# Optimization experiments

Hardware: AMD Instinct MI355X
Metric: run time of the kernel (lower is better)

The kernel has to match this reference:

```python
import jax, jax.numpy as jnp
import numpy as np

# dims (match init_kwargs / input_specs)
B, T = 32, 512
DIM, DEPTH, HEADS, NB_FEAT, N_MASKS = 256, 6, 8, 128, 4
DIM_HEAD = DIM // HEADS  # 32
FF_MULT = 4
KERNEL_EPS = 1e-4


def _orth_proj(key, m, d):
    # FAVOR+ gaussian orthogonal random features: stacked QR blocks, row norms from fresh gaussians
    nb = m // d
    keys = jax.random.split(key, nb + 1)
    blocks = []
    for i in range(nb):
        g = jax.random.normal(keys[i], (d, d))
        q, _ = jnp.linalg.qr(g)
        blocks.append(q.T)
    proj = jnp.concatenate(blocks, axis=0)  # (m, d)
    norms = jnp.linalg.norm(jax.random.normal(keys[-1], (m, d)), axis=-1)
    return (proj * norms[:, None]).astype(jnp.float32)


def setup_inputs() -> dict:
    key = jax.random.key(0)
    ks = jax.random.split(key, 12)
    init = lambda k, sh: (jax.random.normal(k, sh, dtype=jnp.float32) * 0.02)
    L = DEPTH
    return {
        "mel": jax.random.normal(ks[0], (B, DIM, T), dtype=jnp.float32),
        "proj": _orth_proj(ks[1], NB_FEAT, DIM_HEAD),
        "ln1_g": jnp.ones((L, DIM), jnp.float32), "ln1_b": jnp.zeros((L, DIM), jnp.float32),
        "Wq": init(ks[2], (L, DIM, DIM)), "Wk": init(ks[3], (L, DIM, DIM)),
        "Wv": init(ks[4], (L, DIM, DIM)),
        "Wo": init(ks[5], (L, DIM, DIM)), "bo": jnp.zeros((L, DIM), jnp.float32),
        "ln2_g": jnp.ones((L, DIM), jnp.float32), "ln2_b": jnp.zeros((L, DIM), jnp.float32),
        "W1": init(ks[6], (L, DIM, FF_MULT * DIM)), "b1": jnp.zeros((L, FF_MULT * DIM), jnp.float32),
        "W2": init(ks[7], (L, FF_MULT * DIM, DIM)), "b2": jnp.zeros((L, DIM), jnp.float32),
        "Wm": init(ks[8], (DIM, N_MASKS)), "bm": jnp.zeros((N_MASKS,), jnp.float32),
    }


def _ln(x, g, b):
    mu = jnp.mean(x, -1, keepdims=True)
    var = jnp.var(x, -1, keepdims=True)
    return (x - mu) * jax.lax.rsqrt(var + 1e-5) * g + b


def _softmax_kernel(x, proj, is_query):
    # x: (B,H,N,dh), proj: (m,dh)
    dn = x.shape[-1] ** -0.25
    ratio = proj.shape[0] ** -0.5
    xd = jnp.einsum('bhnd,md->bhnm', x * dn, proj)
    diag = 0.5 * jnp.sum(jnp.square(x * dn), axis=-1, keepdims=True)
    if is_query:
        mx = jnp.max(xd, axis=-1, keepdims=True)
    else:
        mx = jnp.max(xd, axis=(-1, -2), keepdims=True)
    return ratio * (jnp.exp(xd - diag - mx) + KERNEL_EPS)


def _split_heads(x):
    b, n, _ = x.shape
    return x.reshape(b, n, HEADS, DIM_HEAD).transpose(0, 2, 1, 3)  # (B,H,N,dh)


def _forward(mel, proj, ln1_g, ln1_b, Wq, Wk, Wv, Wo, bo, ln2_g, ln2_b, W1, b1, W2, b2, Wm, bm):
    x = jnp.transpose(mel, (0, 2, 1))  # (B, T, DIM)
    for l in range(DEPTH):
        # --- FAVOR+ self-attention (pre-LN, non-causal linear attention) ---
        h = _ln(x, ln1_g[l], ln1_b[l])
        q = _split_heads(h @ Wq[l])
        k = _split_heads(h @ Wk[l])
        v = _split_heads(h @ Wv[l])
        qp = _softmax_kernel(q, proj, True)   # (B,H,T,m)
        kp = _softmax_kernel(k, proj, False)  # (B,H,T,m)
        ctx = jnp.einsum('bhnm,bhnd->bhmd', kp, v)          # (B,H,m,dh)
        o = jnp.einsum('bhnm,bhmd->bhnd', qp, ctx)          # (B,H,T,dh)
        denom = jnp.einsum('bhnm,bhm->bhn', qp, kp.sum(axis=2))
        o = o / denom[..., None]
        o = o.transpose(0, 2, 1, 3).reshape(x.shape[0], x.shape[1], DIM)
        x = x + o @ Wo[l] + bo[l]
        h = _ln(x, ln2_g[l], ln2_b[l])
        x = x + jax.nn.gelu(h @ W1[l] + b1[l]) @ W2[l] + b2[l]
    masks = x @ Wm + bm                  # (B, T, M)
    return jnp.transpose(masks, (0, 2, 1))  # (B, M, T)


def reference(mel, proj, ln1_g, ln1_b, Wq, Wk, Wv, Wo, bo, ln2_g, ln2_b, W1, b1, W2, b2, Wm, bm):
    return _forward(mel, proj, ln1_g, ln1_b, Wq, Wk, Wv, Wo, bo, ln2_g, ln2_b, W1, b1, W2, b2, Wm, bm)
```

## Files before the change

kernel.cpp:

```cpp
#include <hip/hip_runtime.h>
#include <math.h>

#define B 32
#define T 512
#define D 256
#define H 8
#define DH 32
#define MF 128
#define NLAYER 6
#define FF 1024
#define NM 4
#define BT (B*T)
#define BH (B*H)

#define DN2H 0.08838834764831845f
#define DNS  0.4204482076268573f
#define RATIO 0.08838834764831845f
#define KEPS 1e-4f

typedef __attribute__((ext_vector_type(8))) short short8;
typedef __attribute__((ext_vector_type(4))) float f32x4;

#define MFMA(a, b, c) __builtin_amdgcn_mfma_f32_16x16x32_bf16(a, b, c, 0, 0, 0)

#define SWZG(l) (((((l) & 3) + (((l) >> 3) & 3)) & 3) * 8)
#define RS(li, gi) (((((gi) - ((li) >> 1)) & 3)) * 8)

#define WAIT_VM(N) asm volatile("s_waitcnt vmcnt(" #N ")" ::: "memory")

__device__ __forceinline__ ushort f2b(float x) {
  union { float f; unsigned u; } c; c.f = x;
  unsigned r = (c.u + 0x7FFFu + ((c.u >> 16) & 1u)) >> 16;
  return (ushort)r;
}
__device__ __forceinline__ float bf2f(ushort u) {
  union { unsigned u; float f; } c; c.u = ((unsigned)u) << 16;
  return c.f;
}
__device__ __forceinline__ void gload16(const ushort* g, ushort* l) {
  __builtin_amdgcn_global_load_lds((const __attribute__((address_space(1))) void*)g,
                                   (__attribute__((address_space(3))) void*)l, 16, 0, 0);
}

__global__ void transpose_mel(const float* __restrict__ mel, float* __restrict__ x) {
  __shared__ float tile[32][33];
  int b = blockIdx.z;
  int d0 = blockIdx.y * 32, t0 = blockIdx.x * 32;
  int tx = threadIdx.x, ty = threadIdx.y;
  #pragma unroll
  for (int i = 0; i < 32; i += 8)
    tile[ty + i][tx] = mel[(b * D + d0 + ty + i) * T + t0 + tx];
  __syncthreads();
  #pragma unroll
  for (int i = 0; i < 32; i += 8)
    x[(b * T + t0 + ty + i) * D + d0 + tx] = tile[tx][ty + i];
}

__global__ void wtrans(const float* __restrict__ W, ushort* __restrict__ WT,
                       int K, int N, size_t lin, size_t lout) {
  __shared__ float tile[32][33];
  int l = blockIdx.z;
  const float* Wl = W + (size_t)l * lin;
  ushort* WTl = WT + (size_t)l * lout;
  int k0 = blockIdx.y * 32, n0 = blockIdx.x * 32;
  int tx = threadIdx.x, ty = threadIdx.y;
  #pragma unroll
  for (int i = 0; i < 32; i += 8)
    tile[ty + i][tx] = Wl[(size_t)(k0 + ty + i) * N + n0 + tx];
  __syncthreads();
  #pragma unroll
  for (int i = 0; i < 32; i += 8)
    WTl[(size_t)(n0 + ty + i) * K + k0 + tx] = f2b(tile[tx][ty + i]);
}

__global__ void proj_conv(const float* __restrict__ proj, ushort* __restrict__ projd) {
  int e = blockIdx.x * 256 + threadIdx.x;
  if (e < MF * DH) projd[e] = f2b(proj[e] * DNS);
}

__global__ __launch_bounds__(256) void ln_kernel(const float* __restrict__ x, const float* __restrict__ g,
                          const float* __restrict__ bb, ushort* __restrict__ y) {
  int row = blockIdx.x * 4 + (threadIdx.x >> 6);
  int lane = threadIdx.x & 63;
  const float4 v = ((const float4*)(x + (size_t)row * D))[lane];
  float s = v.x + v.y + v.z + v.w;
  #pragma unroll
  for (int off = 32; off; off >>= 1) s += __shfl_down(s, off);
  s = __shfl(s, 0);
  float mu = s * (1.0f / 256.0f);
  float dx = v.x - mu, dy = v.y - mu, dz = v.z - mu, dw = v.w - mu;
  float q = dx * dx + dy * dy + dz * dz + dw * dw;
  #pragma unroll
  for (int off = 32; off; off >>= 1) q += __shfl_down(q, off);
  q = __shfl(q, 0);
  float rstd = rsqrtf(q * (1.0f / 256.0f) + 1e-5f);
  const float4 gg = ((const float4*)g)[lane];
  const float4 be = ((const float4*)bb)[lane];
  ushort4 o;
  o.x = f2b(dx * rstd * gg.x + be.x);
  o.y = f2b(dy * rstd * gg.y + be.y);
  o.z = f2b(dz * rstd * gg.z + be.z);
  o.w = f2b(dw * rstd * gg.w + be.w);
  ((ushort4*)(y + (size_t)row * D))[lane] = o;
}

template<int EPI, int BM>
__global__ __launch_bounds__(256) void gemm_bf16(
    const ushort* __restrict__ A, const ushort* __restrict__ BTm,
    const float* __restrict__ bias,
    ushort* __restrict__ outB,
    ushort* __restrict__ qo, ushort* __restrict__ ko, ushort* __restrict__ vT,
    int N, int K) {
  constexpr int MFR = BM / 32;
  __shared__ __align__(16) ushort Al[2][BM * 32];
  __shared__ __align__(16) ushort Bl[2][128 * 32];
  int tid = threadIdx.x;
  int wave = tid >> 6, lane = tid & 63;
  int wr = wave >> 1, wc = wave & 1;
  int gi = lane >> 4, li = lane & 15;
  int lrow = lane >> 2, lkb = SWZG(lane);
  int row0 = blockIdx.y * BM, col0 = blockIdx.x * 128;
  f32x4 acc[MFR][4] = {};

  auto stage = [&](int buf, int kk) {
    #pragma unroll
    for (int i = 0; i < BM / 64; i++) {
      int chunk = wave * (BM / 64) + i;
      gload16(&A[(size_t)(row0 + chunk * 16 + lrow) * K + kk + lkb], &Al[buf][chunk * 512]);
    }
    #pragma unroll
    for (int i = 0; i < 2; i++) {
      int chunk = wave * 2 + i;
      gload16(&BTm[(size_t)(col0 + chunk * 16 + lrow) * K + kk + lkb], &Bl[buf][chunk * 512]);
    }
  };

  stage(0, 0);
  int cur = 0;
  for (int k0 = 0; k0 < K; k0 += 32, cur ^= 1) {
    if (k0 + 32 < K) {
      stage(cur ^ 1, k0 + 32);
      if (BM == 64) { WAIT_VM(3); } else { WAIT_VM(4); }
    } else {
      WAIT_VM(0);
    }
    __builtin_amdgcn_s_barrier();
    __builtin_amdgcn_sched_barrier(0);
    short8 a[MFR], b[4];
    #pragma unroll
    for (int m = 0; m < MFR; m++)
      a[m] = *(const short8*)&Al[cur][(wr * (MFR * 16) + m * 16 + li) * 32 + RS(li, gi)];
    #pragma unroll
    for (int n = 0; n < 4; n++)
      b[n] = *(const short8*)&Bl[cur][(wc * 64 + n * 16 + li) * 32 + RS(li, gi)];
    #pragma unroll
    for (int m = 0; m < MFR; m++)
      #pragma unroll
      for (int n = 0; n < 4; n++)
        acc[m][n] = MFMA(a[m], b[n], acc[m][n]);
    __builtin_amdgcn_s_barrier();
  }
  #pragma unroll
  for (int m = 0; m < MFR; m++) {
    int rbase = row0 + wr * (MFR * 16) + m * 16 + gi * 4;
    #pragma unroll
    for (int n = 0; n < 4; n++) {
      int col = col0 + wc * 64 + n * 16 + li;
      f32x4 v = acc[m][n];
      if (EPI == 2) {
        float bs = bias[col];
        #pragma unroll
        for (int r = 0; r < 4; r++) {
          float u = v[r] + bs;
          float p = u + 0.044715f * u * u * u;
          float gel = u / (1.0f + __expf(-1.5957691216057308f * p));
          outB[(size_t)(rbase + r) * N + col] = f2b(gel);
        }
      } else {
        if (col < 256) {
          #pragma unroll
          for (int r = 0; r < 4; r++) qo[(size_t)(rbase + r) * 256 + col] = f2b(v[r]);
        } else if (col < 512) {
          #pragma unroll
          for (int r = 0; r < 4; r++) ko[(size_t)(rbase + r) * 256 + col - 256] = f2b(v[r]);
        } else {
          int b_ = rbase >> 9, t = rbase & 511;
          int hh = (col - 512) >> 5, d = (col - 512) & 31;
          ushort4 pk;
          pk.x = f2b(v[0]); pk.y = f2b(v[1]); pk.z = f2b(v[2]); pk.w = f2b(v[3]);
          *(ushort4*)&vT[((size_t)((b_ * 8 + hh) * 32 + d)) * 512 + t] = pk;
        }
      }
    }
  }
}

__global__ __launch_bounds__(256) void ctx_fused(
    const ushort* __restrict__ kb, const ushort* __restrict__ projd,
    const ushort* __restrict__ vT, ushort* __restrict__ Bmat) {
  __shared__ __align__(16) ushort Kl[512 * 32];
  __shared__ __align__(16) ushort Pl[128 * 32];
  __shared__ __align__(16) ushort Sl[2][128 * 40];
  __shared__ __align__(16) ushort Bvl[2][32 * 32];
  __shared__ float dg_s[512];
  __shared__ float red_s[256];
  int bh = blockIdx.x;
  int b = bh >> 3, h = bh & 7;
  int tid = threadIdx.x, wave = tid >> 6, lane = tid & 63;
  int gi = lane >> 4, li = lane & 15;
  int lrow = lane >> 2, lkb = (lane & 3) * 8;
  const ushort* Kg = kb + (size_t)(b * 512) * 256 + h * 32;
  const ushort* Vg = vT + (size_t)bh * 32 * 512;
  #pragma unroll
  for (int i = 0; i < 8; i++) {
    int chunk = wave * 8 + i;
    gload16(&Kg[(size_t)(chunk * 16 + lrow) * 256 + lkb], &Kl[chunk * 512]);
  }
  #pragma unroll
  for (int i = 0; i < 2; i++) {
    int chunk = wave * 2 + i;
    gload16(&projd[(chunk * 16 + lrow) * 32 + lkb], &Pl[chunk * 512]);
  }
  __syncthreads();
  #pragma unroll
  for (int i = 0; i < 2; i++) {
    int t = tid * 2 + i;
    const ushort* kr = &Kl[t * 32];
    float s = 0.f;
    #pragma unroll
    for (int j = 0; j < 32; j++) { float v = bf2f(kr[j]); s += v * v; }
    dg_s[t] = DN2H * s;
  }
  short8 bp0 = *(const short8*)&Pl[(wave * 32 + li) * 32 + gi * 8];
  short8 bp1 = *(const short8*)&Pl[(wave * 32 + 16 + li) * 32 + gi * 8];
  float smax = -1e30f;
  for (int c = 0; c < 16; c++) {
    int t0c = c * 32;
    short8 a0 = *(const short8*)&Kl[(t0c + li) * 32 + gi * 8];
    short8 a1 = *(const short8*)&Kl[(t0c + 16 + li) * 32 + gi * 8];
    f32x4 s00 = {}, s01 = {}, s10 = {}, s11 = {};
    s00 = MFMA(a0, bp0, s00); s01 = MFMA(a0, bp1, s01);
    s10 = MFMA(a1, bp0, s10); s11 = MFMA(a1, bp1, s11);
    #pragma unroll
    for (int r = 0; r < 4; r++)
      smax = fmaxf(smax, fmaxf(fmaxf(s00[r], s01[r]), fmaxf(s10[r], s11[r])));
  }
  red_s[tid] = smax;
  __syncthreads();
  for (int s = 128; s; s >>= 1) {
    if (tid < s) red_s[tid] = fmaxf(red_s[tid], red_s[tid + s]);
    __syncthreads();
  }
  float km = red_s[0];
  f32x4 cacc[2][2] = {};
  float ks0 = 0.f, ks1 = 0.f;
  int cur = 0;
  for (int c = 0; c < 16; c++, cur ^= 1) {
    int t0c = c * 32;
    if (wave < 2)
      gload16(&Vg[(size_t)(wave * 16 + lrow) * 512 + t0c + lkb], &Bvl[cur][wave * 512]);
    short8 a0 = *(const short8*)&Kl[(t0c + li) * 32 + gi * 8];
    short8 a1 = *(const short8*)&Kl[(t0c + 16 + li) * 32 + gi * 8];
    f32x4 s00 = {}, s01 = {}, s10 = {}, s11 = {};
    s00 = MFMA(a0, bp0, s00); s01 = MFMA(a0, bp1, s01);
    s10 = MFMA(a1, bp0, s10); s11 = MFMA(a1, bp1, s11);
    ushort4 w00, w01, w10, w11;
    #pragma unroll
    for (int r = 0; r < 4; r++) {
      float d0 = dg_s[t0c + gi * 4 + r];
      float d1 = dg_s[t0c + 16 + gi * 4 + r];
      float k00 = RATIO * (__expf(s00[r] - d0 - km) + KEPS);
      float k01 = RATIO * (__expf(s01[r] - d0 - km) + KEPS);
      float k10 = RATIO * (__expf(s10[r] - d1 - km) + KEPS);
      float k11 = RATIO * (__expf(s11[r] - d1 - km) + KEPS);
      ks0 += k00 + k10; ks1 += k01 + k11;
      ((ushort*)&w00)[r] = f2b(k00); ((ushort*)&w01)[r] = f2b(k01);
      ((ushort*)&w10)[r] = f2b(k10); ((ushort*)&w11)[r] = f2b(k11);
    }
    *(ushort4*)&Sl[cur][(wave * 32 + li) * 40 + gi * 4]           = w00;
    *(ushort4*)&Sl[cur][(wave * 32 + 16 + li) * 40 + gi * 4]      = w01;
    *(ushort4*)&Sl[cur][(wave * 32 + li) * 40 + 16 + gi * 4]      = w10;
    *(ushort4*)&Sl[cur][(wave * 32 + 16 + li) * 40 + 16 + gi * 4] = w11;
    __syncthreads();
    short8 ca0 = *(const short8*)&Sl[cur][(wave * 32 + li) * 40 + gi * 8];
    short8 ca1 = *(const short8*)&Sl[cur][(wave * 32 + 16 + li) * 40 + gi * 8];
    short8 cb0 = *(const short8*)&Bvl[cur][li * 32 + gi * 8];
    short8 cb1 = *(const short8*)&Bvl[cur][(16 + li) * 32 + gi * 8];
    cacc[0][0] = MFMA(ca0, cb0, cacc[0][0]);
    cacc[0][1] = MFMA(ca0, cb1, cacc[0][1]);
    cacc[1][0] = MFMA(ca1, cb0, cacc[1][0]);
    cacc[1][1] = MFMA(ca1, cb1, cacc[1][1]);
  }
  ks0 += __shfl_xor(ks0, 16); ks0 += __shfl_xor(ks0, 32);
  ks1 += __shfl_xor(ks1, 16); ks1 += __shfl_xor(ks1, 32);
  if (gi == 0) {
    Bmat[((size_t)bh * 48 + 32) * 128 + wave * 32 + li] = f2b(ks0);
    Bmat[((size_t)bh * 48 + 32) * 128 + wave * 32 + 16 + li] = f2b(ks1);
  }
  #pragma unroll
  for (int m = 0; m < 2; m++)
    #pragma unroll
    for (int n = 0; n < 2; n++) {
      int dd = n * 16 + li;
      int mg = wave * 32 + m * 16 + gi * 4;
      ushort4 pk;
      pk.x = f2b(cacc[m][n][0]); pk.y = f2b(cacc[m][n][1]);
      pk.z = f2b(cacc[m][n][2]); pk.w = f2b(cacc[m][n][3]);
      *(ushort4*)&Bmat[((size_t)bh * 48 + dd) * 128 + mg] = pk;
    }
  for (int e = tid; e < 15 * 128; e += 256)
    Bmat[((size_t)bh * 48 + 33) * 128 + e] = 0;
}

__global__ __launch_bounds__(256) void favq_o(
    const ushort* __restrict__ qb, const ushort* __restrict__ projd,
    const ushort* __restrict__ Bmat, ushort* __restrict__ ob) {
  __shared__ __align__(16) ushort Ql[64 * 32];
  __shared__ __align__(16) ushort Pl[128 * 32];
  __shared__ __align__(16) ushort Sl[64 * 136];
  __shared__ __align__(16) ushort Bml[48 * 136];
  __shared__ float dgq[64];
  int bh = blockIdx.y;
  int t0 = blockIdx.x * 64;
  int b = bh >> 3, h = bh & 7;
  int tid = threadIdx.x, wave = tid >> 6, lane = tid & 63;
  int gi = lane >> 4, li = lane & 15;
  int lrow = lane >> 2, lkb = (lane & 3) * 8;
  const ushort* Qg = qb + (size_t)(b * 512) * 256 + h * 32;
  gload16(&Qg[(size_t)(t0 + wave * 16 + lrow) * 256 + lkb], &Ql[wave * 512]);
  #pragma unroll
  for (int i = 0; i < 2; i++) {
    int chunk = wave * 2 + i;
    gload16(&projd[(chunk * 16 + lrow) * 32 + lkb], &Pl[chunk * 512]);
  }
  #pragma unroll
  for (int j = 0; j < 3; j++) {
    int c = j * 256 + tid;
    int r = c >> 4, g = c & 15;
    *(uint4*)&Bml[r * 136 + g * 8] = *(const uint4*)&Bmat[(size_t)bh * 48 * 128 + r * 128 + g * 8];
  }
  __syncthreads();
  if (tid < 64) {
    const ushort* qr = &Ql[tid * 32];
    float s = 0.f;
    #pragma unroll
    for (int j = 0; j < 32; j++) { float v = bf2f(qr[j]); s += v * v; }
    dgq[tid] = DN2H * s;
  }
  short8 bq = *(const short8*)&Ql[(wave * 16 + li) * 32 + gi * 8];
  f32x4 sacc[8] = {};
  #pragma unroll
  for (int m = 0; m < 8; m++) {
    short8 a = *(const short8*)&Pl[(m * 16 + li) * 32 + gi * 8];
    sacc[m] = MFMA(a, bq, sacc[m]);
  }
  __syncthreads();
  float mx = -1e30f;
  #pragma unroll
  for (int m = 0; m < 8; m++)
    #pragma unroll
    for (int r = 0; r < 4; r++) mx = fmaxf(mx, sacc[m][r]);
  mx = fmaxf(mx, __shfl_xor(mx, 16));
  mx = fmaxf(mx, __shfl_xor(mx, 32));
  float dg = dgq[wave * 16 + li];
  #pragma unroll
  for (int m = 0; m < 8; m++) {
    ushort4 o4;
    #pragma unroll
    for (int r = 0; r < 4; r++)
      ((ushort*)&o4)[r] = f2b(RATIO * (__expf(sacc[m][r] - dg - mx) + KEPS));
    *(ushort4*)&Sl[(wave * 16 + li) * 136 + m * 16 + gi * 4] = o4;
  }
  __syncthreads();
  f32x4 oacc[3] = {};
  #pragma unroll
  for (int ks = 0; ks < 4; ks++) {
    short8 a = *(const short8*)&Sl[(wave * 16 + li) * 136 + ks * 32 + gi * 8];
    #pragma unroll
    for (int n = 0; n < 3; n++) {
      short8 bb = *(const short8*)&Bml[(n * 16 + li) * 136 + ks * 32 + gi * 8];
      oacc[n] = MFMA(a, bb, oacc[n]);
    }
  }
  int t = t0 + wave * 16 + gi * 4;
  float den[4];
  #pragma unroll
  for (int r = 0; r < 4; r++) den[r] = __shfl(oacc[2][r], lane & 48);
  #pragma unroll
  for (int n = 0; n < 2; n++)
    #pragma unroll
    for (int r = 0; r < 4; r++)
      ob[((size_t)(b * 512) + t + r) * 256 + h * 32 + n * 16 + li] = f2b(oacc[n][r] / den[r]);
}

__global__ __launch_bounds__(256) void wo_ff1(
    const ushort* __restrict__ ob, const ushort* __restrict__ woT,
    const float* __restrict__ bo, const float* __restrict__ res, float* __restrict__ x,
    const float* __restrict__ g, const float* __restrict__ bvec,
    const ushort* __restrict__ w1T, const float* __restrict__ b1v,
    ushort* __restrict__ ffh) {
  __shared__ __align__(16) ushort Al[2][32 * 32];
  __shared__ __align__(16) ushort Bl[2][256 * 32];
  __shared__ __align__(16) ushort Hp[8 * 1024];
  __shared__ float rs1[4 * 32], rs2[4 * 32];
  int tid = threadIdx.x, wave = tid >> 6, lane = tid & 63;
  int gi = lane >> 4, li = lane & 15;
  int lrow = lane >> 2, lkb = SWZG(lane);
  int row0 = blockIdx.x * 32;
  int wc = wave;
  f32x4 acc[2][4] = {};

  auto stage1 = [&](int buf, int kk) {
    if (wave < 2)
      gload16(&ob[(size_t)(row0 + wave * 16 + lrow) * 256 + kk + lkb], &Al[buf][wave * 512]);
    #pragma unroll
    for (int i = 0; i < 4; i++) {
      int chunk = wave * 4 + i;
      gload16(&woT[(size_t)(chunk * 16 + lrow) * 256 + kk + lkb], &Bl[buf][chunk * 512]);
    }
  };
  stage1(0, 0);
  __syncthreads();
  int cur = 0;
  for (int k0 = 0; k0 < 256; k0 += 32, cur ^= 1) {
    if (k0 + 32 < 256) stage1(cur ^ 1, k0 + 32);
    short8 a[2], b[4];
    #pragma unroll
    for (int m = 0; m < 2; m++)
      a[m] = *(const short8*)&Al[cur][(m * 16 + li) * 32 + RS(li, gi)];
    #pragma unroll
    for (int n = 0; n < 4; n++)
      b[n] = *(const short8*)&Bl[cur][(wc * 64 + n * 16 + li) * 32 + RS(li, gi)];
    #pragma unroll
    for (int m = 0; m < 2; m++)
      #pragma unroll
      for (int n = 0; n < 4; n++)
        acc[m][n] = MFMA(a[m], b[n], acc[m][n]);
    __syncthreads();
  }
  #pragma unroll
  for (int m = 0; m < 2; m++) {
    #pragma unroll
    for (int r = 0; r < 4; r++) {
      int row = row0 + m * 16 + gi * 4 + r;
      int ridx = m * 16 + gi * 4 + r;
      float s1 = 0.f, s2 = 0.f;
      #pragma unroll
      for (int n = 0; n < 4; n++) {
        int col = wc * 64 + n * 16 + li;
        float val = acc[m][n][r] + bo[col] + res[(size_t)row * 256 + col];
        acc[m][n][r] = val;
        s1 += val; s2 += val * val;
      }
      #pragma unroll
      for (int off = 1; off <= 8; off <<= 1) { s1 += __shfl_xor(s1, off); s2 += __shfl_xor(s2, off); }
      if (li == 0) { rs1[wave * 32 + ridx] = s1; rs2[wave * 32 + ridx] = s2; }
    }
  }
  __syncthreads();
  {
    float g4[4], bv4[4];
    #pragma unroll
    for (int n = 0; n < 4; n++) {
      int col = wc * 64 + n * 16 + li;
      g4[n] = g[col]; bv4[n] = bvec[col];
    }
    #pragma unroll
    for (int m = 0; m < 2; m++) {
      #pragma unroll
      for (int r = 0; r < 4; r++) {
        int row32 = m * 16 + gi * 4 + r;
        int row = row0 + row32;
        float t1 = rs1[row32] + rs1[32 + row32] + rs1[64 + row32] + rs1[96 + row32];
        float t2 = rs2[row32] + rs2[32 + row32] + rs2[64 + row32] + rs2[96 + row32];
        float mu = t1 * (1.f / 256.f);
        float rstd = rsqrtf(t2 * (1.f / 256.f) - mu * mu + 1e-5f);
        #pragma unroll
        for (int n = 0; n < 4; n++) {
          int col = wc * 64 + n * 16 + li;
          float val = acc[m][n][r];
          x[(size_t)row * 256 + col] = val;
          float hv = (val - mu) * rstd * g4[n] + bv4[n];
          int kc = col >> 5, c32 = col & 31;
          int G = c32 >> 3, c7 = c32 & 7;
          int slot = (G - (row32 >> 1)) & 3;
          Hp[kc * 1024 + row32 * 32 + slot * 8 + c7] = f2b(hv);
        }
      }
    }
  }
  auto stage2 = [&](int buf, int st) {
    int nc = st >> 3, ks = st & 7;
    #pragma unroll
    for (int i = 0; i < 4; i++) {
      int chunk = wave * 4 + i;
      gload16(&w1T[(size_t)(nc * 256 + chunk * 16 + lrow) * 256 + ks * 32 + lkb], &Bl[buf][chunk * 512]);
    }
  };
  stage2(0, 0);
  __syncthreads();
  cur = 0;
  f32x4 fac[2][4] = {};
  for (int st = 0; st < 32; st++, cur ^= 1) {
    int nc = st >> 3, ks = st & 7;
    if (st + 1 < 32) stage2(cur ^ 1, st + 1);
    short8 a[2], b[4];
    #pragma unroll
    for (int m = 0; m < 2; m++)
      a[m] = *(const short8*)&Hp[ks * 1024 + (m * 16 + li) * 32 + RS(li, gi)];
    #pragma unroll
    for (int n = 0; n < 4; n++)
      b[n] = *(const short8*)&Bl[cur][(wc * 64 + n * 16 + li) * 32 + RS(li, gi)];
    #pragma unroll
    for (int m = 0; m < 2; m++)
      #pragma unroll
      for (int n = 0; n < 4; n++)
        fac[m][n] = MFMA(a[m], b[n], fac[m][n]);
    if (ks == 7) {
      #pragma unroll
      for (int m = 0; m < 2; m++) {
        int rbase = row0 + m * 16 + gi * 4;
        #pragma unroll
        for (int n = 0; n < 4; n++) {
          int col = nc * 256 + wc * 64 + n * 16 + li;
          float bs = b1v[col];
          #pragma unroll
          for (int r = 0; r < 4; r++) {
            float u = fac[m][n][r] + bs;
            float p = u + 0.044715f * u * u * u;
            float gel = u / (1.0f + __expf(-1.5957691216057308f * p));
            ffh[(size_t)(rbase + r) * 1024 + col] = f2b(gel);
            fac[m][n][r] = 0.f;
          }
        }
      }
    }
    __syncthreads();
  }
}

__global__ __launch_bounds__(256) void ff2_qkv(
    const ushort* __restrict__ ffh, const ushort* __restrict__ w2T,
    const float* __restrict__ b2v, const float* __restrict__ res, float* __restrict__ x,
    const float* __restrict__ g, const float* __restrict__ bvec,
    const ushort* __restrict__ qkvT,
    ushort* __restrict__ qo, ushort* __restrict__ ko, ushort* __restrict__ vT) {
  __shared__ __align__(16) ushort Al[2][32 * 32];
  __shared__ __align__(16) ushort Bl[2][256 * 32];
  __shared__ __align__(16) ushort Hp[8 * 1024];
  __shared__ float rs1[4 * 32], rs2[4 * 32];
  int tid = threadIdx.x, wave = tid >> 6, lane = tid & 63;
  int gi = lane >> 4, li = lane & 15;
  int lrow = lane >> 2, lkb = SWZG(lane);
  int row0 = blockIdx.x * 32;
  int wc = wave;
  f32x4 acc[2][4] = {};

  auto stage1 = [&](int buf, int kk) {
    if (wave < 2)
      gload16(&ffh[(size_t)(row0 + wave * 16 + lrow) * 1024 + kk + lkb], &Al[buf][wave * 512]);
    #pragma unroll
    for (int i = 0; i < 4; i++) {
      int chunk = wave * 4 + i;
      gload16(&w2T[(size_t)(chunk * 16 + lrow) * 1024 + kk + lkb], &Bl[buf][chunk * 512]);
    }
  };
  stage1(0, 0);
  __syncthreads();
  int cur = 0;
  for (int k0 = 0; k0 < 1024; k0 += 32, cur ^= 1) {
    if (k0 + 32 < 1024) stage1(cur ^ 1, k0 + 32);
    short8 a[2], b[4];
    #pragma unroll
    for (int m = 0; m < 2; m++)
      a[m] = *(const short8*)&Al[cur][(m * 16 + li) * 32 + RS(li, gi)];
    #pragma unroll
    for (int n = 0; n < 4; n++)
      b[n] = *(const short8*)&Bl[cur][(wc * 64 + n * 16 + li) * 32 + RS(li, gi)];
    #pragma unroll
    for (int m = 0; m < 2; m++)
      #pragma unroll
      for (int n = 0; n < 4; n++)
        acc[m][n] = MFMA(a[m], b[n], acc[m][n]);
    __syncthreads();
  }
  #pragma unroll
  for (int m = 0; m < 2; m++) {
    #pragma unroll
    for (int r = 0; r < 4; r++) {
      int row = row0 + m * 16 + gi * 4 + r;
      int ridx = m * 16 + gi * 4 + r;
      float s1 = 0.f, s2 = 0.f;
      #pragma unroll
      for (int n = 0; n < 4; n++) {
        int col = wc * 64 + n * 16 + li;
        float val = acc[m][n][r] + b2v[col] + res[(size_t)row * 256 + col];
        acc[m][n][r] = val;
        s1 += val; s2 += val * val;
      }
      #pragma unroll
      for (int off = 1; off <= 8; off <<= 1) { s1 += __shfl_xor(s1, off); s2 += __shfl_xor(s2, off); }
      if (li == 0) { rs1[wave * 32 + ridx] = s1; rs2[wave * 32 + ridx] = s2; }
    }
  }
  __syncthreads();
  {
    float g4[4], bv4[4];
    #pragma unroll
    for (int n = 0; n < 4; n++) {
      int col = wc * 64 + n * 16 + li;
      g4[n] = g[col]; bv4[n] = bvec[col];
    }
    #pragma unroll
    for (int m = 0; m < 2; m++) {
      #pragma unroll
      for (int r = 0; r < 4; r++) {
        int row32 = m * 16 + gi * 4 + r;
        int row = row0 + row32;
        float t1 = rs1[row32] + rs1[32 + row32] + rs1[64 + row32] + rs1[96 + row32];
        float t2 = rs2[row32] + rs2[32 + row32] + rs2[64 + row32] + rs2[96 + row32];
        float mu = t1 * (1.f / 256.f);
        float rstd = rsqrtf(t2 * (1.f / 256.f) - mu * mu + 1e-5f);
        #pragma unroll
        for (int n = 0; n < 4; n++) {
          int col = wc * 64 + n * 16 + li;
          float val = acc[m][n][r];
          x[(size_t)row * 256 + col] = val;
          float hv = (val - mu) * rstd * g4[n] + bv4[n];
          int kc = col >> 5, c32 = col & 31;
          int G = c32 >> 3, c7 = c32 & 7;
          int slot = (G - (row32 >> 1)) & 3;
          Hp[kc * 1024 + row32 * 32 + slot * 8 + c7] = f2b(hv);
        }
      }
    }
  }
  auto stage2 = [&](int buf, int st) {
    int nc = st >> 3, ks = st & 7;
    #pragma unroll
    for (int i = 0; i < 4; i++) {
      int chunk = wave * 4 + i;
      gload16(&qkvT[(size_t)(nc * 256 + chunk * 16 + lrow) * 256 + ks * 32 + lkb], &Bl[buf][chunk * 512]);
    }
  };
  stage2(0, 0);
  __syncthreads();
  cur = 0;
  f32x4 fac[2][4] = {};
  for (int st = 0; st < 24; st++, cur ^= 1) {
    int nc = st >> 3, ks = st & 7;
    if (st + 1 < 24) stage2(cur ^ 1, st + 1);
    short8 a[2], b[4];
    #pragma unroll
    for (int m = 0; m < 2; m++)
      a[m] = *(const short8*)&Hp[ks * 1024 + (m * 16 + li) * 32 + RS(li, gi)];
    #pragma unroll
    for (int n = 0; n < 4; n++)
      b[n] = *(const short8*)&Bl[cur][(wc * 64 + n * 16 + li) * 32 + RS(li, gi)];
    #pragma unroll
    for (int m = 0; m < 2; m++)
      #pragma unroll
      for (int n = 0; n < 4; n++)
        fac[m][n] = MFMA(a[m], b[n], fac[m][n]);
    if (ks == 7) {
      #pragma unroll
      for (int m = 0; m < 2; m++) {
        int rbase = row0 + m * 16 + gi * 4;
        #pragma unroll
        for (int n = 0; n < 4; n++) {
          int col256 = wc * 64 + n * 16 + li;
          if (nc == 0) {
            #pragma unroll
            for (int r = 0; r < 4; r++) { qo[(size_t)(rbase + r) * 256 + col256] = f2b(fac[m][n][r]); fac[m][n][r] = 0.f; }
          } else if (nc == 1) {
            #pragma unroll
            for (int r = 0; r < 4; r++) { ko[(size_t)(rbase + r) * 256 + col256] = f2b(fac[m][n][r]); fac[m][n][r] = 0.f; }
          } else {
            int b_ = rbase >> 9, t = rbase & 511;
            int hh = col256 >> 5, d = col256 & 31;
            ushort4 pk;
            pk.x = f2b(fac[m][n][0]); pk.y = f2b(fac[m][n][1]);
            pk.z = f2b(fac[m][n][2]); pk.w = f2b(fac[m][n][3]);
            *(ushort4*)&vT[((size_t)((b_ * 8 + hh) * 32 + d)) * 512 + t] = pk;
            fac[m][n][0] = fac[m][n][1] = fac[m][n][2] = fac[m][n][3] = 0.f;
          }
        }
      }
    }
    __syncthreads();
  }
}

__global__ __launch_bounds__(256) void gemm_mask(
    const ushort* __restrict__ A, const ushort* __restrict__ BTm,
    const float* __restrict__ bias, const float* __restrict__ res,
    const float* __restrict__ Wm, const float* __restrict__ bm, float* __restrict__ mout,
    int K) {
  __shared__ __align__(16) ushort Al[2][32 * 32];
  __shared__ __align__(16) ushort Bl[2][256 * 32];
  __shared__ float pmS[4 * 128];
  int tid = threadIdx.x, wave = tid >> 6, lane = tid & 63;
  int gi = lane >> 4, li = lane & 15;
  int lrow = lane >> 2, lkb = SWZG(lane);
  int row0 = blockIdx.x * 32;
  int wc = wave;
  f32x4 acc[2][4] = {};

  auto stage = [&](int buf, int kk) {
    if (wave < 2)
      gload16(&A[(size_t)(row0 + wave * 16 + lrow) * K + kk + lkb], &Al[buf][wave * 512]);
    #pragma unroll
    for (int i = 0; i < 4; i++) {
      int chunk = wave * 4 + i;
      gload16(&BTm[(size_t)(chunk * 16 + lrow) * K + kk + lkb], &Bl[buf][chunk * 512]);
    }
  };
  stage(0, 0);
  __syncthreads();
  int cur = 0;
  for (int k0 = 0; k0 < K; k0 += 32, cur ^= 1) {
    if (k0 + 32 < K) stage(cur ^ 1, k0 + 32);
    short8 a[2], b[4];
    #pragma unroll
    for (int m = 0; m < 2; m++)
      a[m] = *(const short8*)&Al[cur][(m * 16 + li) * 32 + RS(li, gi)];
    #pragma unroll
    for (int n = 0; n < 4; n++)
      b[n] = *(const short8*)&Bl[cur][(wc * 64 + n * 16 + li) * 32 + RS(li, gi)];
    #pragma unroll
    for (int m = 0; m < 2; m++)
      #pragma unroll
      for (int n = 0; n < 4; n++)
        acc[m][n] = MFMA(a[m], b[n], acc[m][n]);
    __syncthreads();
  }
  #pragma unroll
  for (int m = 0; m < 2; m++) {
    #pragma unroll
    for (int r = 0; r < 4; r++) {
      int row = row0 + m * 16 + gi * 4 + r;
      int ridx = m * 16 + gi * 4 + r;
      #pragma unroll
      for (int n = 0; n < 4; n++) {
        int col = wc * 64 + n * 16 + li;
        acc[m][n][r] += bias[col] + res[(size_t)row * 256 + col];
      }
      #pragma unroll
      for (int msk = 0; msk < NM; msk++) {
        float sm = 0.f;
        #pragma unroll
        for (int n = 0; n < 4; n++) {
          int col = wc * 64 + n * 16 + li;
          sm += acc[m][n][r] * Wm[col * NM + msk];
        }
        #pragma unroll
        for (int off = 1; off <= 8; off <<= 1) sm += __shfl_xor(sm, off);
        if (li == 0) pmS[wave * 128 + ridx * 4 + msk] = sm;
      }
    }
  }
  __syncthreads();
  if (tid < 128) {
    int ridx = tid >> 2, msk = tid & 3;
    float tot = pmS[ridx * 4 + msk] + pmS[128 + ridx * 4 + msk] +
                pmS[256 + ridx * 4 + msk] + pmS[384 + ridx * 4 + msk];
    int grow = row0 + ridx;
    int bb_ = grow >> 9, t = grow & 511;
    mout[((size_t)(bb_ * NM) + msk) * 512 + t] = tot + bm[msk];
  }
}

extern "C" void kernel_launch(void* const* d_in, const int* in_sizes, int n_in,
                              void* d_out, int out_size, void* d_ws, size_t ws_size,
                              hipStream_t stream) {
  const float* mel   = (const float*)d_in[0];
  const float* proj  = (const float*)d_in[1];
  const float* ln1_g = (const float*)d_in[2];
  const float* ln1_b = (const float*)d_in[3];
  const float* Wq    = (const float*)d_in[4];
  const float* Wk    = (const float*)d_in[5];
  const float* Wv    = (const float*)d_in[6];
  const float* Wo    = (const float*)d_in[7];
  const float* bo    = (const float*)d_in[8];
  const float* ln2_g = (const float*)d_in[9];
  const float* ln2_b = (const float*)d_in[10];
  const float* W1    = (const float*)d_in[11];
  const float* b1    = (const float*)d_in[12];
  const float* W2    = (const float*)d_in[13];
  const float* b2    = (const float*)d_in[14];
  const float* Wm    = (const float*)d_in[15];
  const float* bm    = (const float*)d_in[16];

  float* x      = (float*)d_ws;
  ushort* us    = (ushort*)(x + (size_t)BT * D);
  ushort* h     = us;                   us += (size_t)BT * D;
  ushort* qb    = us;                   us += (size_t)BT * D;
  ushort* kb    = us;                   us += (size_t)BT * D;
  ushort* vT    = us;                   us += (size_t)BH * 32 * T;
  ushort* ob    = us;                   us += (size_t)BT * D;
  ushort* ffh   = us;                   us += (size_t)BT * FF;
  ushort* Bmat  = us;                   us += (size_t)BH * 48 * MF;
  ushort* qkvT  = us;                   us += (size_t)NLAYER * 768 * 256;
  ushort* woT   = us;                   us += (size_t)NLAYER * 256 * 256;
  ushort* w1T   = us;                   us += (size_t)NLAYER * 1024 * 256;
  ushort* w2T   = us;                   us += (size_t)NLAYER * 256 * 1024;
  ushort* projd = us;                   us += (size_t)MF * DH;

  wtrans<<<dim3(8, 8, NLAYER), dim3(32, 8), 0, stream>>>(Wq, qkvT, 256, 256, 65536, 768 * 256);
  wtrans<<<dim3(8, 8, NLAYER), dim3(32, 8), 0, stream>>>(Wk, qkvT + 256 * 256, 256, 256, 65536, 768 * 256);
  wtrans<<<dim3(8, 8, NLAYER), dim3(32, 8), 0, stream>>>(Wv, qkvT + 512 * 256, 256, 256, 65536, 768 * 256);
  wtrans<<<dim3(8, 8, NLAYER), dim3(32, 8), 0, stream>>>(Wo, woT, 256, 256, 65536, 65536);
  wtrans<<<dim3(32, 8, NLAYER), dim3(32, 8), 0, stream>>>(W1, w1T, 256, 1024, 262144, 262144);
  wtrans<<<dim3(8, 32, NLAYER), dim3(32, 8), 0, stream>>>(W2, w2T, 1024, 256, 262144, 262144);
  proj_conv<<<16, 256, 0, stream>>>(proj, projd);

  transpose_mel<<<dim3(T / 32, D / 32, B), dim3(32, 8), 0, stream>>>(mel, x);
  ln_kernel<<<BT / 4, 256, 0, stream>>>(x, ln1_g, ln1_b, h);

  gemm_bf16<0, 64><<<dim3(6, 256), 256, 0, stream>>>(h, qkvT,
      nullptr, nullptr, qb, kb, vT, 768, 256);

  for (int l = 0; l < NLAYER; l++) {
    ctx_fused<<<BH, 256, 0, stream>>>(kb, projd, vT, Bmat);
    favq_o<<<dim3(8, BH), 256, 0, stream>>>(qb, projd, Bmat, ob);
    wo_ff1<<<BT / 32, 256, 0, stream>>>(ob, woT + (size_t)l * 256 * 256,
        bo + l * D, x, x, ln2_g + l * D, ln2_b + l * D,
        w1T + (size_t)l * 1024 * 256, b1 + (size_t)l * FF, ffh);
    if (l < NLAYER - 1) {
      ff2_qkv<<<BT / 32, 256, 0, stream>>>(ffh, w2T + (size_t)l * 256 * 1024,
          b2 + l * D, x, x, ln1_g + (l + 1) * D, ln1_b + (l + 1) * D,
          qkvT + (size_t)(l + 1) * 768 * 256, qb, kb, vT);
    } else {
      gemm_mask<<<BT / 32, 256, 0, stream>>>(ffh, w2T + (size_t)l * 256 * 1024,
          b2 + l * D, x, Wm, bm, (float*)d_out, 1024);
    }
  }
}
```

Before: 724.7 us.

## Use per-wave private LDS staging to drop block barriers in fused GEMM loops

```diff
diff --git a/kernel.cpp b/kernel.cpp
--- a/kernel.cpp
+++ b/kernel.cpp
@@ -399,44 +399,42 @@
     const float* __restrict__ g, const float* __restrict__ bvec,
     const ushort* __restrict__ w1T, const float* __restrict__ b1v,
     ushort* __restrict__ ffh) {
-  __shared__ __align__(16) ushort Al[2][32 * 32];
-  __shared__ __align__(16) ushort Bl[2][256 * 32];
+  __shared__ __align__(16) ushort Apr[4][2][1024];
+  __shared__ __align__(16) ushort Bpr[4][2][2048];
   __shared__ __align__(16) ushort Hp[8 * 1024];
   __shared__ float rs1[4 * 32], rs2[4 * 32];
   int tid = threadIdx.x, wave = tid >> 6, lane = tid & 63;
   int gi = lane >> 4, li = lane & 15;
   int lrow = lane >> 2, lkb = SWZG(lane);
   int row0 = blockIdx.x * 32;
-  int wc = wave;
   f32x4 acc[2][4] = {};
 
   auto stage1 = [&](int buf, int kk) {
-    if (wave < 2)
-      gload16(&ob[(size_t)(row0 + wave * 16 + lrow) * 256 + kk + lkb], &Al[buf][wave * 512]);
-    #pragma unroll
-    for (int i = 0; i < 4; i++) {
-      int chunk = wave * 4 + i;
-      gload16(&woT[(size_t)(chunk * 16 + lrow) * 256 + kk + lkb], &Bl[buf][chunk * 512]);
-    }
+    #pragma unroll
+    for (int i = 0; i < 2; i++)
+      gload16(&ob[(size_t)(row0 + i * 16 + lrow) * 256 + kk + lkb], &Apr[wave][buf][i * 512]);
+    #pragma unroll
+    for (int i = 0; i < 4; i++)
+      gload16(&woT[(size_t)(wave * 64 + i * 16 + lrow) * 256 + kk + lkb], &Bpr[wave][buf][i * 512]);
   };
   stage1(0, 0);
-  __syncthreads();
   int cur = 0;
   for (int k0 = 0; k0 < 256; k0 += 32, cur ^= 1) {
-    if (k0 + 32 < 256) stage1(cur ^ 1, k0 + 32);
+    if (k0 + 32 < 256) { stage1(cur ^ 1, k0 + 32); WAIT_VM(6); }
+    else { WAIT_VM(0); }
+    __builtin_amdgcn_sched_barrier(0);
     short8 a[2], b[4];
     #pragma unroll
     for (int m = 0; m < 2; m++)
-      a[m] = *(const short8*)&Al[cur][(m * 16 + li) * 32 + RS(li, gi)];
+      a[m] = *(const short8*)&Apr[wave][cur][(m * 16 + li) * 32 + RS(li, gi)];
     #pragma unroll
     for (int n = 0; n < 4; n++)
-      b[n] = *(const short8*)&Bl[cur][(wc * 64 + n * 16 + li) * 32 + RS(li, gi)];
+      b[n] = *(const short8*)&Bpr[wave][cur][(n * 16 + li) * 32 + RS(li, gi)];
     #pragma unroll
     for (int m = 0; m < 2; m++)
       #pragma unroll
       for (int n = 0; n < 4; n++)
         acc[m][n] = MFMA(a[m], b[n], acc[m][n]);
-    __syncthreads();
   }
   #pragma unroll
   for (int m = 0; m < 2; m++) {
@@ -447,7 +445,7 @@
       float s1 = 0.f, s2 = 0.f;
       #pragma unroll
       for (int n = 0; n < 4; n++) {
-        int col = wc * 64 + n * 16 + li;
+        int col = wave * 64 + n * 16 + li;
         float val = acc[m][n][r] + bo[col] + res[(size_t)row * 256 + col];
         acc[m][n][r] = val;
         s1 += val; s2 += val * val;
@@ -462,7 +460,7 @@
     float g4[4], bv4[4];
     #pragma unroll
     for (int n = 0; n < 4; n++) {
-      int col = wc * 64 + n * 16 + li;
+      int col = wave * 64 + n * 16 + li;
       g4[n] = g[col]; bv4[n] = bvec[col];
     }
     #pragma unroll
@@ -477,7 +475,7 @@
         float rstd = rsqrtf(t2 * (1.f / 256.f) - mu * mu + 1e-5f);
         #pragma unroll
         for (int n = 0; n < 4; n++) {
-          int col = wc * 64 + n * 16 + li;
+          int col = wave * 64 + n * 16 + li;
           float val = acc[m][n][r];
           x[(size_t)row * 256 + col] = val;
           float hv = (val - mu) * rstd * g4[n] + bv4[n];
@@ -492,10 +490,9 @@
   auto stage2 = [&](int buf, int st) {
     int nc = st >> 3, ks = st & 7;
     #pragma unroll
-    for (int i = 0; i < 4; i++) {
-      int chunk = wave * 4 + i;
-      gload16(&w1T[(size_t)(nc * 256 + chunk * 16 + lrow) * 256 + ks * 32 + lkb], &Bl[buf][chunk * 512]);
-    }
+    for (int i = 0; i < 4; i++)
+      gload16(&w1T[(size_t)(nc * 256 + wave * 64 + i * 16 + lrow) * 256 + ks * 32 + lkb],
+              &Bpr[wave][buf][i * 512]);
   };
   stage2(0, 0);
   __syncthreads();
@@ -503,14 +500,16 @@
   f32x4 fac[2][4] = {};
   for (int st = 0; st < 32; st++, cur ^= 1) {
     int nc = st >> 3, ks = st & 7;
-    if (st + 1 < 32) stage2(cur ^ 1, st + 1);
+    if (st + 1 < 32) { stage2(cur ^ 1, st + 1); WAIT_VM(4); }
+    else { WAIT_VM(0); }
+    __builtin_amdgcn_sched_barrier(0);
     short8 a[2], b[4];
     #pragma unroll
     for (int m = 0; m < 2; m++)
       a[m] = *(const short8*)&Hp[ks * 1024 + (m * 16 + li) * 32 + RS(li, gi)];
     #pragma unroll
     for (int n = 0; n < 4; n++)
-      b[n] = *(const short8*)&Bl[cur][(wc * 64 + n * 16 + li) * 32 + RS(li, gi)];
+      b[n] = *(const short8*)&Bpr[wave][cur][(n * 16 + li) * 32 + RS(li, gi)];
     #pragma unroll
     for (int m = 0; m < 2; m++)
       #pragma unroll
@@ -522,7 +521,7 @@
         int rbase = row0 + m * 16 + gi * 4;
         #pragma unroll
         for (int n = 0; n < 4; n++) {
-          int col = nc * 256 + wc * 64 + n * 16 + li;
+          int col = nc * 256 + wave * 64 + n * 16 + li;
           float bs = b1v[col];
           #pragma unroll
           for (int r = 0; r < 4; r++) {
@@ -535,7 +534,6 @@
         }
       }
     }
-    __syncthreads();
   }
 }
 
@@ -545,44 +543,42 @@
     const float* __restrict__ g, const float* __restrict__ bvec,
     const ushort* __restrict__ qkvT,
     ushort* __restrict__ qo, ushort* __restrict__ ko, ushort* __restrict__ vT) {
-  __shared__ __align__(16) ushort Al[2][32 * 32];
-  __shared__ __align__(16) ushort Bl[2][256 * 32];
+  __shared__ __align__(16) ushort Apr[4][2][1024];
+  __shared__ __align__(16) ushort Bpr[4][2][2048];
   __shared__ __align__(16) ushort Hp[8 * 1024];
   __shared__ float rs1[4 * 32], rs2[4 * 32];
   int tid = threadIdx.x, wave = tid >> 6, lane = tid & 63;
   int gi = lane >> 4, li = lane & 15;
   int lrow = lane >> 2, lkb = SWZG(lane);
   int row0 = blockIdx.x * 32;
-  int wc = wave;
   f32x4 acc[2][4] = {};
 
   auto stage1 = [&](int buf, int kk) {
-    if (wave < 2)
-      gload16(&ffh[(size_t)(row0 + wave * 16 + lrow) * 1024 + kk + lkb], &Al[buf][wave * 512]);
-    #pragma unroll
-    for (int i = 0; i < 4; i++) {
-      int chunk = wave * 4 + i;
-      gload16(&w2T[(size_t)(chunk * 16 + lrow) * 1024 + kk + lkb], &Bl[buf][chunk * 512]);
-    }
+    #pragma unroll
+    for (int i = 0; i < 2; i++)
+      gload16(&ffh[(size_t)(row0 + i * 16 + lrow) * 1024 + kk + lkb], &Apr[wave][buf][i * 512]);
+    #pragma unroll
+    for (int i = 0; i < 4; i++)
+      gload16(&w2T[(size_t)(wave * 64 + i * 16 + lrow) * 1024 + kk + lkb], &Bpr[wave][buf][i * 512]);
   };
   stage1(0, 0);
-  __syncthreads();
   int cur = 0;
   for (int k0 = 0; k0 < 1024; k0 += 32, cur ^= 1) {
-    if (k0 + 32 < 1024) stage1(cur ^ 1, k0 + 32);
+    if (k0 + 32 < 1024) { stage1(cur ^ 1, k0 + 32); WAIT_VM(6); }
+    else { WAIT_VM(0); }
+    __builtin_amdgcn_sched_barrier(0);
     short8 a[2], b[4];
     #pragma unroll
     for (int m = 0; m < 2; m++)
-      a[m] = *(const short8*)&Al[cur][(m * 16 + li) * 32 + RS(li, gi)];
+      a[m] = *(const short8*)&Apr[wave][cur][(m * 16 + li) * 32 + RS(li, gi)];
     #pragma unroll
     for (int n = 0; n < 4; n++)
-      b[n] = *(const short8*)&Bl[cur][(wc * 64 + n * 16 + li) * 32 + RS(li, gi)];
+      b[n] = *(const short8*)&Bpr[wave][cur][(n * 16 + li) * 32 + RS(li, gi)];
     #pragma unroll
     for (int m = 0; m < 2; m++)
       #pragma unroll
       for (int n = 0; n < 4; n++)
         acc[m][n] = MFMA(a[m], b[n], acc[m][n]);
-    __syncthreads();
   }
   #pragma unroll
   for (int m = 0; m < 2; m++) {
@@ -593,7 +589,7 @@
       float s1 = 0.f, s2 = 0.f;
       #pragma unroll
       for (int n = 0; n < 4; n++) {
-        int col = wc * 64 + n * 16 + li;
+        int col = wave * 64 + n * 16 + li;
         float val = acc[m][n][r] + b2v[col] + res[(size_t)row * 256 + col];
         acc[m][n][r] = val;
         s1 += val; s2 += val * val;
@@ -608,7 +604,7 @@
     float g4[4], bv4[4];
     #pragma unroll
     for (int n = 0; n < 4; n++) {
-      int col = wc * 64 + n * 16 + li;
+      int col = wave * 64 + n * 16 + li;
       g4[n] = g[col]; bv4[n] = bvec[col];
     }
     #pragma unroll
@@ -623,7 +619,7 @@
         float rstd = rsqrtf(t2 * (1.f / 256.f) - mu * mu + 1e-5f);
         #pragma unroll
         for (int n = 0; n < 4; n++) {
-          int col = wc * 64 + n * 16 + li;
+          int col = wave * 64 + n * 16 + li;
           float val = acc[m][n][r];
           x[(size_t)row * 256 + col] = val;
           float hv = (val - mu) * rstd * g4[n] + bv4[n];
@@ -638,10 +634,9 @@
   auto stage2 = [&](int buf, int st) {
     int nc = st >> 3, ks = st & 7;
     #pragma unroll
-    for (int i = 0; i < 4; i++) {
-      int chunk = wave * 4 + i;
-      gload16(&qkvT[(size_t)(nc * 256 + chunk * 16 + lrow) * 256 + ks * 32 + lkb], &Bl[buf][chunk * 512]);
-    }
+    for (int i = 0; i < 4; i++)
+      gload16(&qkvT[(size_t)(nc * 256 + wave * 64 + i * 16 + lrow) * 256 + ks * 32 + lkb],
+              &Bpr[wave][buf][i * 512]);
   };
   stage2(0, 0);
   __syncthreads();
@@ -649,14 +644,16 @@
   f32x4 fac[2][4] = {};
   for (int st = 0; st < 24; st++, cur ^= 1) {
     int nc = st >> 3, ks = st & 7;
-    if (st + 1 < 24) stage2(cur ^ 1, st + 1);
+    if (st + 1 < 24) { stage2(cur ^ 1, st + 1); WAIT_VM(4); }
+    else { WAIT_VM(0); }
+    __builtin_amdgcn_sched_barrier(0);
     short8 a[2], b[4];
     #pragma unroll
     for (int m = 0; m < 2; m++)
       a[m] = *(const short8*)&Hp[ks * 1024 + (m * 16 + li) * 32 + RS(li, gi)];
     #pragma unroll
     for (int n = 0; n < 4; n++)
-      b[n] = *(const short8*)&Bl[cur][(wc * 64 + n * 16 + li) * 32 + RS(li, gi)];
+      b[n] = *(const short8*)&Bpr[wave][cur][(n * 16 + li) * 32 + RS(li, gi)];
     #pragma unroll
     for (int m = 0; m < 2; m++)
       #pragma unroll
@@ -668,7 +665,7 @@
         int rbase = row0 + m * 16 + gi * 4;
         #pragma unroll
         for (int n = 0; n < 4; n++) {
-          int col256 = wc * 64 + n * 16 + li;
+          int col256 = wave * 64 + n * 16 + li;
           if (nc == 0) {
             #pragma unroll
             for (int r = 0; r < 4; r++) { qo[(size_t)(rbase + r) * 256 + col256] = f2b(fac[m][n][r]); fac[m][n][r] = 0.f; }
@@ -687,7 +684,6 @@
         }
       }
     }
-    __syncthreads();
   }
 }
 
```

After: 698.9 us, median of 4. 3.6% less time.
